# Performance work log

Measured on AMD Instinct MI355X. Metric: run time of the kernel, lower is better.

Reference implementation:

```python
import jax, jax.numpy as jnp
import numpy as np


def _rope(x, token_positions, theta):
    # x: [B, H, S, D], token_positions: [S]
    d = x.shape[-1]
    freqs = 1.0 / theta ** (jnp.arange(0, d, 2, dtype=jnp.float32) / d)  # [D/2]
    angles = token_positions.astype(jnp.float32)[:, None] * freqs[None, :]  # [S, D/2]
    cos, sin = jnp.cos(angles), jnp.sin(angles)
    x_even = x[..., 0::2]
    x_odd = x[..., 1::2]
    new_even = x_even * cos - x_odd * sin
    new_odd = x_even * sin + x_odd * cos
    return jnp.stack([new_even, new_odd], axis=-1).reshape(x.shape)


def setup_inputs() -> dict:
    key = jax.random.key(0)
    ks = jax.random.split(key, 5)
    B, S, D = 2, 2048, 1024
    scale = 1.0 / np.sqrt(D)
    return {
        "x": jax.random.normal(ks[0], (B, S, D), dtype=jnp.float32),
        "Wq": jax.random.normal(ks[1], (D, D), dtype=jnp.float32) * scale,
        "Wk": jax.random.normal(ks[2], (D, D), dtype=jnp.float32) * scale,
        "Wv": jax.random.normal(ks[3], (D, D), dtype=jnp.float32) * scale,
        "Wo": jax.random.normal(ks[4], (D, D), dtype=jnp.float32) * scale,
        "token_positions": jnp.arange(S, dtype=jnp.int32),
        "rope_theta": 10000,
    }


def reference(x, Wq, Wk, Wv, Wo, token_positions, rope_theta):
    B, S, Dm = x.shape
    H = 16
    d_k = Dm // H
    # nn.Linear(bias=False): y = x @ W.T
    def proj(W):
        y = jnp.einsum('bsd,ed->bse', x, W)
        return y.reshape(B, S, H, d_k).transpose(0, 2, 1, 3)  # [B,H,S,Dk]
    q = _rope(proj(Wq), token_positions, float(rope_theta))
    k = _rope(proj(Wk), token_positions, float(rope_theta))
    v = proj(Wv)
    scores = jnp.einsum('bhqd,bhkd->bhqk', q, k) / jnp.sqrt(jnp.float32(d_k))
    causal = jnp.tril(jnp.ones((S, S), dtype=bool))
    scores = jnp.where(causal, scores, -jnp.inf)
    p = jax.nn.softmax(scores, axis=-1)
    vals = jnp.einsum('bhqk,bhkd->bhqd', p, v)
    out = vals.transpose(0, 2, 1, 3).reshape(B, S, Dm)
    return jnp.einsum('bsd,ed->bse', out, Wo)
```

## Files before the change

### kernel.cpp

```cpp
#include <hip/hip_runtime.h>
#include <hip/hip_bf16.h>
#include <stdint.h>

typedef __attribute__((ext_vector_type(8))) __bf16 bf16x8;
typedef __attribute__((ext_vector_type(4))) float f32x4;
typedef __hip_bfloat16 bf16;

#define GLDS(g, l) __builtin_amdgcn_global_load_lds( \
    (const __attribute__((address_space(1))) void*)(g), \
    (__attribute__((address_space(3))) void*)(l), 16, 0, 0)

#define SCALE_Q 0.18033688f
#define MFIX 12.0f

#define OFF_XB     ((size_t)0)
#define OFF_WQKVB  ((size_t)8388608)
#define OFF_WOB    ((size_t)14680064)
#define OFF_QB     ((size_t)16777216)
#define OFF_KB     ((size_t)25165824)
#define OFF_VTB    ((size_t)33554432)
#define OFF_CS     ((size_t)41943040)
#define OFF_SN     ((size_t)42205184)

__global__ void prep_kernel(const float* __restrict__ x, const float* __restrict__ wq,
                            const float* __restrict__ wk, const float* __restrict__ wv,
                            const float* __restrict__ wo,
                            bf16* __restrict__ xb, bf16* __restrict__ wqkvb,
                            bf16* __restrict__ wob,
                            const int* __restrict__ pos, const void* __restrict__ theta_p,
                            float* __restrict__ cst, float* __restrict__ snt)
{
    const int region = blockIdx.y;
    if (region == 5) {
        if (blockIdx.x >= 256) return;
        const int t = blockIdx.x * 256 + threadIdx.x;
        const int s = t >> 5, i = t & 31;
        const int ti = ((const int*)theta_p)[0];
        const float theta = (ti > 0 && ti < 100000000) ? (float)ti : ((const float*)theta_p)[0];
        const float fr = expf(-(float)i * (1.0f / 32.0f) * logf(theta));
        const float ang = (float)pos[s] * fr;
        cst[t] = cosf(ang);
        snt[t] = sinf(ang);
        return;
    }
    const float* src;
    bf16* dst;
    int count;
    switch (region) {
        case 0:  src = x;  dst = xb;              count = 4096 * 1024; break;
        case 1:  src = wq; dst = wqkvb;           count = 1024 * 1024; break;
        case 2:  src = wk; dst = wqkvb + 1048576; count = 1024 * 1024; break;
        case 3:  src = wv; dst = wqkvb + 2097152; count = 1024 * 1024; break;
        default: src = wo; dst = wob;             count = 1024 * 1024; break;
    }
    const int i = (blockIdx.x * 256 + threadIdx.x) * 4;
    if (i >= count) return;
    const float4 v = *(const float4*)(src + i);
    union { bf16 h[4]; short4 s4; } u;
    u.h[0] = __float2bfloat16(v.x);
    u.h[1] = __float2bfloat16(v.y);
    u.h[2] = __float2bfloat16(v.z);
    u.h[3] = __float2bfloat16(v.w);
    *(short4*)(dst + i) = u.s4;
}

template<int MODE, int BM>
__global__ __launch_bounds__(256) void gemm_bt(
    const bf16* __restrict__ A, const bf16* __restrict__ B,
    const int K, const int N,
    float* __restrict__ outf,
    bf16* __restrict__ qb, bf16* __restrict__ kb, bf16* __restrict__ vtb,
    const float* __restrict__ cst, const float* __restrict__ snt)
{
    constexpr int NF = BM / 32;
    constexpr int AG = BM / 64;
    constexpr int ABYTES = BM * 64;
    constexpr int BBYTES = 128 * 64;
    constexpr int DBSZ = 2 * (ABYTES + BBYTES);
    constexpr int TLSZ = (MODE == 0) ? 128 * 130 * 2 : 0;
    constexpr int POOL = DBSZ > TLSZ ? DBSZ : TLSZ;
    __shared__ __align__(16) char smem[POOL];
    const int tid = threadIdx.x;
    const int wave = tid >> 6, lane = tid & 63;
    const int lr = lane & 15, lk = lane >> 4;

    const int nwg = gridDim.x * gridDim.y;
    const int flat = blockIdx.y * gridDim.x + blockIdx.x;
    const int wg = (flat & 7) * (nwg >> 3) + (flat >> 3);
    const int m0 = (wg % gridDim.x) * BM;
    const int n0 = (wg / gridDim.x) * 128;

    const int wm = (wave >> 1) * (BM / 2);
    const int wn = (wave & 1) * 64;
    const int srow = tid >> 2, sseg = tid & 3;
    const int swel = (sseg ^ ((srow + (srow >> 2)) & 3)) * 8;

    f32x4 acc[NF][4] = {};

    const bf16* aRow = A + (size_t)(m0 + srow) * K + swel;
    const bf16* bRow = B + (size_t)(n0 + srow) * K + swel;
    const size_t rowK64 = (size_t)64 * K;

    auto STAGE = [&](int step, int c) {
        char* lA = smem + c * ABYTES + tid * 16;
        char* lB = smem + 2 * ABYTES + c * BBYTES + tid * 16;
        const int off = step * 32;
#pragma unroll
        for (int g = 0; g < AG; ++g)
            GLDS(aRow + off + (size_t)g * rowK64, lA + g * 4096);
#pragma unroll
        for (int g = 0; g < 2; ++g)
            GLDS(bRow + off + (size_t)g * rowK64, lB + g * 4096);
    };

    const int xoff = (lk ^ ((lr + (lr >> 2)) & 3)) << 4;
    const int NSTEP = K >> 5;

    STAGE(0, 0);

    for (int ks = 0; ks < NSTEP; ++ks) {
        const int c = ks & 1;
        if (ks < NSTEP - 1) {
            STAGE(ks + 1, c ^ 1);
            if constexpr (AG == 2) asm volatile("s_waitcnt vmcnt(4)" ::: "memory");
            else                   asm volatile("s_waitcnt vmcnt(3)" ::: "memory");
        } else {
            asm volatile("s_waitcnt vmcnt(0)" ::: "memory");
        }
        __builtin_amdgcn_s_barrier();
        __builtin_amdgcn_sched_barrier(0);
        const char* aBase = smem + c * ABYTES;
        const char* bBase = smem + 2 * ABYTES + c * BBYTES;

        bf16x8 af[NF], bfr[4];
#pragma unroll
        for (int i = 0; i < NF; ++i)
            af[i] = *(const bf16x8*)(aBase + (wm + i * 16 + lr) * 64 + xoff);
#pragma unroll
        for (int j = 0; j < 4; ++j)
            bfr[j] = *(const bf16x8*)(bBase + (wn + j * 16 + lr) * 64 + xoff);
#pragma unroll
        for (int i = 0; i < NF; ++i)
#pragma unroll
            for (int j = 0; j < 4; ++j)
                acc[i][j] = __builtin_amdgcn_mfma_f32_16x16x32_bf16(af[i], bfr[j], acc[i][j], 0, 0, 0);
        __builtin_amdgcn_sched_barrier(0);
        __builtin_amdgcn_s_barrier();
    }

    if constexpr (MODE == 1) {
#pragma unroll
        for (int i = 0; i < NF; ++i)
#pragma unroll
            for (int j = 0; j < 4; ++j)
#pragma unroll
                for (int r = 0; r < 4; ++r) {
                    const int row = m0 + wm + i * 16 + lk * 4 + r;
                    const int col = n0 + wn + j * 16 + lr;
                    outf[(size_t)row * N + col] = acc[i][j][r];
                }
    } else {
        const int matn = n0 >> 10;
        if (matn == 2) {
            bf16* Tl = (bf16*)smem;
#pragma unroll
            for (int i = 0; i < NF; ++i)
#pragma unroll
                for (int j = 0; j < 4; ++j)
#pragma unroll
                    for (int r = 0; r < 4; ++r) {
                        const int trow = wm + i * 16 + lk * 4 + r;
                        const int tcol = wn + j * 16 + lr;
                        Tl[tcol * 130 + trow] = __float2bfloat16(acc[i][j][r]);
                    }
            __syncthreads();
            const int b = m0 >> 11;
            const int s0 = m0 & 2047;
#pragma unroll
            for (int k = 0; k < 8; ++k) {
                const int c = wave * 32 + k * 4 + (lane >> 4);
                const int e = (n0 + c) & 1023;
                const size_t bhi = (size_t)(b * 16 + (e >> 6));
                bf16* dst = vtb + (bhi * 64 + (e & 63)) * 2048 + s0 + lr * 8;
                *(uint4*)dst = *(const uint4*)&Tl[c * 130 + lr * 8];
            }
        } else {
#pragma unroll
            for (int i = 0; i < NF; ++i)
#pragma unroll
                for (int j = 0; j < 4; ++j)
#pragma unroll
                    for (int r = 0; r < 4; ++r) {
                        const int row = m0 + wm + i * 16 + lk * 4 + r;
                        const int col = n0 + wn + j * 16 + lr;
                        float v = acc[i][j][r];
                        float p = __shfl_xor(v, 1);
                        const int e = col & 1023;
                        const int h = e >> 6;
                        const int dd = e & 63;
                        const int b = row >> 11;
                        const int s = row & 2047;
                        const size_t bhi = (size_t)(b * 16 + h);
                        const float cs = cst[s * 32 + (dd >> 1)];
                        const float sn = snt[s * 32 + (dd >> 1)];
                        const float rv = (dd & 1) ? (p * sn + v * cs) : (v * cs - p * sn);
                        if (matn == 0)
                            qb[(bhi * 2048 + s) * 64 + dd] = __float2bfloat16(rv * SCALE_Q);
                        else
                            kb[(bhi * 2048 + s) * 64 + dd] = __float2bfloat16(rv);
                    }
        }
    }
}

__global__ __launch_bounds__(256) void attn_kernel(
    const bf16* __restrict__ qb, const bf16* __restrict__ kb,
    const bf16* __restrict__ vtb, bf16* __restrict__ attnb)
{
    __shared__ __align__(16) bf16 Kl[2][64 * 64];
    __shared__ __align__(16) bf16 Vl[2][64 * 64];
    __shared__ __align__(16) bf16 Pl[4][2][16][72];
    const int tid = threadIdx.x;
    const int wave = tid >> 6, lane = tid & 63;
    const int lr = lane & 15, lk = lane >> 4;
    const int tA = blockIdx.x;
    const int tB = 31 - tA;
    const int bh = blockIdx.y;
    const int qA = tA * 64 + wave * 16;
    const int qB = tB * 64 + wave * 16;

    const bf16* Qp = qb + (size_t)bh * 2048 * 64;
    const bf16* Kp = kb + (size_t)bh * 2048 * 64;
    const bf16* Vp = vtb + (size_t)bh * 64 * 2048;

    const int srow = tid >> 3;
    const int sseg = tid & 7;
    const int sw16 = (sseg ^ (srow & 7)) * 16;
    const char* kg = (const char*)Kp + (size_t)srow * 128 + sw16;
    const char* vg = (const char*)Vp + (size_t)srow * 4096 + sw16;

#define STAGE(kt_, c_) do {                                              \
        const char* kgt = kg + (size_t)(kt_) * 8192;                     \
        GLDS(kgt,              &Kl[c_][0] + tid * 8);                    \
        GLDS(kgt + 32 * 128,   &Kl[c_][0] + 2048 + tid * 8);             \
        const char* vgt = vg + (size_t)(kt_) * 128;                      \
        GLDS(vgt,              &Vl[c_][0] + tid * 8);                    \
        GLDS(vgt + 32 * 4096,  &Vl[c_][0] + 2048 + tid * 8);             \
    } while (0)

    bf16x8 qfA[2], qfB[2];
#pragma unroll
    for (int ks = 0; ks < 2; ++ks) {
        qfA[ks] = *(const bf16x8*)(Qp + (qA + lr) * 64 + ks * 32 + lk * 8);
        qfB[ks] = *(const bf16x8*)(Qp + (qB + lr) * 64 + ks * 32 + lk * 8);
    }

    float sA = 0.f, sB = 0.f;
    f32x4 oA[4] = {}, oB[4] = {};

    STAGE(0, 0);

    const int xoff = (lr & 7) * 8;

    for (int kt = 0; kt <= tB; ++kt) {
        const int c = kt & 1;
        const int kv0 = kt * 64;
        const bool doA = (kt <= tA);
        if (kt < tB) {
            STAGE(kt + 1, c ^ 1);
            asm volatile("s_waitcnt vmcnt(4)" ::: "memory");
        } else {
            asm volatile("s_waitcnt vmcnt(0)" ::: "memory");
        }
        __builtin_amdgcn_s_barrier();
        __builtin_amdgcn_sched_barrier(0);
        const bf16* Kc = &Kl[c][0];
        const bf16* Vc = &Vl[c][0];

        f32x4 scB[4] = {}, scA[4] = {};
#pragma unroll
        for (int ks = 0; ks < 2; ++ks) {
            bf16x8 kf[4];
#pragma unroll
            for (int j = 0; j < 4; ++j)
                kf[j] = *(const bf16x8*)(Kc + (j * 16 + lr) * 64 + ((ks * 32 + lk * 8) ^ xoff));
            __builtin_amdgcn_s_setprio(1);
#pragma unroll
            for (int j = 0; j < 4; ++j)
                scB[j] = __builtin_amdgcn_mfma_f32_16x16x32_bf16(kf[j], qfB[ks], scB[j], 0, 0, 0);
            if (doA) {
#pragma unroll
                for (int j = 0; j < 4; ++j)
                    scA[j] = __builtin_amdgcn_mfma_f32_16x16x32_bf16(kf[j], qfA[ks], scA[j], 0, 0, 0);
            }
            __builtin_amdgcn_s_setprio(0);
        }

        bf16x8 vf[2][4];
#pragma unroll
        for (int ks = 0; ks < 2; ++ks)
#pragma unroll
            for (int j = 0; j < 4; ++j)
                vf[ks][j] = *(const bf16x8*)(Vc + (j * 16 + lr) * 64 + ((ks * 32 + lk * 8) ^ xoff));

        auto smx = [&](f32x4* sc, float& ssum, int qX, bool diag, int st) {
            if (diag) {
#pragma unroll
                for (int j = 0; j < 4; ++j)
#pragma unroll
                    for (int r = 0; r < 4; ++r)
                        if (kv0 + j * 16 + lk * 4 + r > qX + lr) sc[j][r] = -1e30f;
            }
            float l0 = 0.f, l1 = 0.f, l2 = 0.f, l3 = 0.f;
#pragma unroll
            for (int j = 0; j < 4; ++j) {
                float pv[4];
                pv[0] = exp2f(sc[j][0] - MFIX);
                pv[1] = exp2f(sc[j][1] - MFIX);
                pv[2] = exp2f(sc[j][2] - MFIX);
                pv[3] = exp2f(sc[j][3] - MFIX);
                l0 += pv[0]; l1 += pv[1]; l2 += pv[2]; l3 += pv[3];
                union { bf16 h[4]; ushort4 s4; } u;
#pragma unroll
                for (int r = 0; r < 4; ++r) u.h[r] = __float2bfloat16(pv[r]);
                *(ushort4*)(&Pl[wave][st][lr][j * 16 + lk * 4]) = u.s4;
            }
            ssum += (l0 + l1) + (l2 + l3);
        };
        auto pv = [&](f32x4* o, int st) {
#pragma unroll
            for (int ks = 0; ks < 2; ++ks) {
                const bf16x8 pf = *(const bf16x8*)(&Pl[wave][st][lr][ks * 32 + lk * 8]);
                __builtin_amdgcn_s_setprio(1);
#pragma unroll
                for (int j = 0; j < 4; ++j)
                    o[j] = __builtin_amdgcn_mfma_f32_16x16x32_bf16(vf[ks][j], pf, o[j], 0, 0, 0);
                __builtin_amdgcn_s_setprio(0);
            }
        };

        smx(scB, sB, qB, kt == tB, 1);
        if (doA) smx(scA, sA, qA, kt == tA, 0);
        pv(oB, 1);
        if (doA) pv(oA, 0);

        __builtin_amdgcn_sched_barrier(0);
        __builtin_amdgcn_s_barrier();
    }

    const int b = bh >> 4, h = bh & 15;
    auto epi = [&](float ssum, f32x4* o, int qX) {
        float s = ssum;
        s += __shfl_xor(s, 16);
        s += __shfl_xor(s, 32);
        const float inv = 1.0f / s;
        const int qq = qX + lr;
        bf16* dst = attnb + (size_t)(b * 2048 + qq) * 1024 + h * 64 + lk * 4;
#pragma unroll
        for (int j = 0; j < 4; ++j) {
            union { bf16 h4[4]; ushort4 s4; } u;
#pragma unroll
            for (int r = 0; r < 4; ++r) u.h4[r] = __float2bfloat16(o[j][r] * inv);
            *(ushort4*)(dst + j * 16) = u.s4;
        }
    };
    epi(sA, oA, qA);
    epi(sB, oB, qB);
#undef STAGE
}

extern "C" void kernel_launch(void* const* d_in, const int* in_sizes, int n_in,
                              void* d_out, int out_size, void* d_ws, size_t ws_size,
                              hipStream_t stream)
{
    const float* x   = (const float*)d_in[0];
    const float* wq  = (const float*)d_in[1];
    const float* wk  = (const float*)d_in[2];
    const float* wv  = (const float*)d_in[3];
    const float* wo  = (const float*)d_in[4];
    const int*   pos = (const int*)d_in[5];
    const void* theta = d_in[6];

    char* ws = (char*)d_ws;
    bf16* xb    = (bf16*)(ws + OFF_XB);
    bf16* attnb = (bf16*)(ws + OFF_XB);
    bf16* wqkvb = (bf16*)(ws + OFF_WQKVB);
    bf16* wob   = (bf16*)(ws + OFF_WOB);
    bf16* qb    = (bf16*)(ws + OFF_QB);
    bf16* kb    = (bf16*)(ws + OFF_KB);
    bf16* vtb   = (bf16*)(ws + OFF_VTB);
    float* cst  = (float*)(ws + OFF_CS);
    float* snt  = (float*)(ws + OFF_SN);

    prep_kernel<<<dim3(4096, 6), 256, 0, stream>>>(x, wq, wk, wv, wo, xb, wqkvb, wob,
                                                   pos, theta, cst, snt);
    gemm_bt<0, 128><<<dim3(32, 24), 256, 0, stream>>>(xb, wqkvb, 1024, 3072, nullptr,
                                                      qb, kb, vtb, cst, snt);
    attn_kernel<<<dim3(16, 32), 256, 0, stream>>>(qb, kb, vtb, attnb);
    gemm_bt<1, 64><<<dim3(64, 8), 256, 0, stream>>>(attnb, wob, 1024, 1024, (float*)d_out,
                                                    nullptr, nullptr, nullptr, nullptr, nullptr);
}
```

Measured before the change: 131.6 us.

## Switch attention to 32x32x16 MFMA with register-resident P via lane shuffles

Rewrites the attention inner loop to use 32x32x16 bf16 MFMA tiles, packing the two causal-paired query tiles (A and B) into the 32 columns of one MFMA instead of issuing separate 16x16 MFMAs for each. The probability matrix is no longer staged through shared memory. It is packed to bf16 with v_cvt_pk_bf16_f32 and rearranged between lane halves with shuffles. Tile A's columns are masked to zero via a bias once A is past its diagonal, so MFMA work for the masked-out half is still issued. This removes the LDS round-trip and its shared buffer but adds shuffle traffic and more accumulator registers.

```diff
diff --git a/kernel.cpp b/kernel.cpp
--- a/kernel.cpp
+++ b/kernel.cpp
@@ -4,6 +4,7 @@
 
 typedef __attribute__((ext_vector_type(8))) __bf16 bf16x8;
 typedef __attribute__((ext_vector_type(4))) float f32x4;
+typedef __attribute__((ext_vector_type(16))) float f32x16;
 typedef __hip_bfloat16 bf16;
 
 #define GLDS(g, l) __builtin_amdgcn_global_load_lds( \
@@ -21,6 +22,12 @@
 #define OFF_VTB    ((size_t)33554432)
 #define OFF_CS     ((size_t)41943040)
 #define OFF_SN     ((size_t)42205184)
+
+static __device__ __forceinline__ unsigned pkbf(float a, float b) {
+    unsigned r;
+    asm("v_cvt_pk_bf16_f32 %0, %1, %2" : "=v"(r) : "v"(a), "v"(b));
+    return r;
+}
 
 __global__ void prep_kernel(const float* __restrict__ x, const float* __restrict__ wq,
                             const float* __restrict__ wk, const float* __restrict__ wv,
@@ -219,15 +226,14 @@
 {
     __shared__ __align__(16) bf16 Kl[2][64 * 64];
     __shared__ __align__(16) bf16 Vl[2][64 * 64];
-    __shared__ __align__(16) bf16 Pl[4][2][16][72];
     const int tid = threadIdx.x;
     const int wave = tid >> 6, lane = tid & 63;
-    const int lr = lane & 15, lk = lane >> 4;
+    const int c32 = lane & 31, G = lane >> 5;
     const int tA = blockIdx.x;
     const int tB = 31 - tA;
     const int bh = blockIdx.y;
-    const int qA = tA * 64 + wave * 16;
-    const int qB = tB * 64 + wave * 16;
+    const int qrow = (c32 < 16) ? (tB * 64 + wave * 16 + c32)
+                                : (tA * 64 + wave * 16 + c32 - 16);
 
     const bf16* Qp = qb + (size_t)bh * 2048 * 64;
     const bf16* Kp = kb + (size_t)bh * 2048 * 64;
@@ -248,24 +254,21 @@
         GLDS(vgt + 32 * 4096,  &Vl[c_][0] + 2048 + tid * 8);             \
     } while (0)
 
-    bf16x8 qfA[2], qfB[2];
-#pragma unroll
-    for (int ks = 0; ks < 2; ++ks) {
-        qfA[ks] = *(const bf16x8*)(Qp + (qA + lr) * 64 + ks * 32 + lk * 8);
-        qfB[ks] = *(const bf16x8*)(Qp + (qB + lr) * 64 + ks * 32 + lk * 8);
-    }
-
-    float sA = 0.f, sB = 0.f;
-    f32x4 oA[4] = {}, oB[4] = {};
+    bf16x8 qf[4];
+#pragma unroll
+    for (int s = 0; s < 4; ++s)
+        qf[s] = *(const bf16x8*)(Qp + (size_t)qrow * 64 + s * 16 + G * 8);
+
+    float ssum = 0.f;
+    f32x16 o0 = {}, o1 = {};
 
     STAGE(0, 0);
 
-    const int xoff = (lr & 7) * 8;
+    const int x7 = c32 & 7;
 
     for (int kt = 0; kt <= tB; ++kt) {
         const int c = kt & 1;
         const int kv0 = kt * 64;
-        const bool doA = (kt <= tA);
         if (kt < tB) {
             STAGE(kt + 1, c ^ 1);
             asm volatile("s_waitcnt vmcnt(4)" ::: "memory");
@@ -277,95 +280,102 @@
         const bf16* Kc = &Kl[c][0];
         const bf16* Vc = &Vl[c][0];
 
-        f32x4 scB[4] = {}, scA[4] = {};
-#pragma unroll
-        for (int ks = 0; ks < 2; ++ks) {
-            bf16x8 kf[4];
-#pragma unroll
-            for (int j = 0; j < 4; ++j)
-                kf[j] = *(const bf16x8*)(Kc + (j * 16 + lr) * 64 + ((ks * 32 + lk * 8) ^ xoff));
+        bf16x8 kf0[4], kf1[4];
+#pragma unroll
+        for (int s = 0; s < 4; ++s) {
+            const int seg = ((2 * s + G) ^ x7) * 8;
+            kf0[s] = *(const bf16x8*)(Kc + (0 * 32 + c32) * 64 + seg);
+            kf1[s] = *(const bf16x8*)(Kc + (1 * 32 + c32) * 64 + seg);
+        }
+
+        f32x16 p0 = {}, p1 = {};
+        __builtin_amdgcn_s_setprio(1);
+#pragma unroll
+        for (int s = 0; s < 4; ++s) {
+            p0 = __builtin_amdgcn_mfma_f32_32x32x16_bf16(kf0[s], qf[s], p0, 0, 0, 0);
+            p1 = __builtin_amdgcn_mfma_f32_32x32x16_bf16(kf1[s], qf[s], p1, 0, 0, 0);
+        }
+        __builtin_amdgcn_s_setprio(0);
+
+        bf16x8 vf0[4], vf1[4];
+#pragma unroll
+        for (int s = 0; s < 4; ++s) {
+            const int seg = ((2 * s + G) ^ x7) * 8;
+            vf0[s] = *(const bf16x8*)(Vc + (0 * 32 + c32) * 64 + seg);
+            vf1[s] = *(const bf16x8*)(Vc + (1 * 32 + c32) * 64 + seg);
+        }
+
+        if (kt == tA || kt == tB) {
+            const int thr0 = qrow - kv0 - 4 * G;
+            const int thr1 = thr0 - 32;
+#pragma unroll
+            for (int r = 0; r < 16; ++r) {
+                const int cr = (r & 3) + 8 * (r >> 2);
+                if (cr > thr0) p0[r] = -1e30f;
+                if (cr > thr1) p1[r] = -1e30f;
+            }
+        }
+        const float bias = (c32 >= 16 && kt > tA) ? -1e30f : -MFIX;
+
+        float ls = 0.f;
+#pragma unroll
+        for (int r = 0; r < 16; ++r) {
+            p0[r] = exp2f(p0[r] + bias);
+            p1[r] = exp2f(p1[r] + bias);
+            ls += p0[r] + p1[r];
+        }
+        ssum += ls;
+
+#pragma unroll
+        for (int s = 0; s < 4; ++s) {
+            const int sb = (s & 1) * 8;
+            float a0, a1, a2, a3, b0, b1, b2, b3;
+            if (s < 2) {
+                a0 = p0[sb+0]; a1 = p0[sb+1]; a2 = p0[sb+2]; a3 = p0[sb+3];
+                b0 = p0[sb+4]; b1 = p0[sb+5]; b2 = p0[sb+6]; b3 = p0[sb+7];
+            } else {
+                a0 = p1[sb+0]; a1 = p1[sb+1]; a2 = p1[sb+2]; a3 = p1[sb+3];
+                b0 = p1[sb+4]; b1 = p1[sb+5]; b2 = p1[sb+6]; b3 = p1[sb+7];
+            }
+            const unsigned plo0 = pkbf(a0, a1), plo1 = pkbf(a2, a3);
+            const unsigned phi0 = pkbf(b0, b1), phi1 = pkbf(b2, b3);
+            const unsigned send0 = G ? plo0 : phi0;
+            const unsigned send1 = G ? plo1 : phi1;
+            const unsigned recv0 = (unsigned)__shfl_xor((int)send0, 32);
+            const unsigned recv1 = (unsigned)__shfl_xor((int)send1, 32);
+            union { unsigned u[4]; bf16x8 v; } pf;
+            pf.u[0] = G ? recv0 : plo0;
+            pf.u[1] = G ? recv1 : plo1;
+            pf.u[2] = G ? phi0 : recv0;
+            pf.u[3] = G ? phi1 : recv1;
             __builtin_amdgcn_s_setprio(1);
-#pragma unroll
-            for (int j = 0; j < 4; ++j)
-                scB[j] = __builtin_amdgcn_mfma_f32_16x16x32_bf16(kf[j], qfB[ks], scB[j], 0, 0, 0);
-            if (doA) {
-#pragma unroll
-                for (int j = 0; j < 4; ++j)
-                    scA[j] = __builtin_amdgcn_mfma_f32_16x16x32_bf16(kf[j], qfA[ks], scA[j], 0, 0, 0);
-            }
+            o0 = __builtin_amdgcn_mfma_f32_32x32x16_bf16(vf0[s], pf.v, o0, 0, 0, 0);
+            o1 = __builtin_amdgcn_mfma_f32_32x32x16_bf16(vf1[s], pf.v, o1, 0, 0, 0);
             __builtin_amdgcn_s_setprio(0);
         }
-
-        bf16x8 vf[2][4];
-#pragma unroll
-        for (int ks = 0; ks < 2; ++ks)
-#pragma unroll
-            for (int j = 0; j < 4; ++j)
-                vf[ks][j] = *(const bf16x8*)(Vc + (j * 16 + lr) * 64 + ((ks * 32 + lk * 8) ^ xoff));
-
-        auto smx = [&](f32x4* sc, float& ssum, int qX, bool diag, int st) {
-            if (diag) {
-#pragma unroll
-                for (int j = 0; j < 4; ++j)
-#pragma unroll
-                    for (int r = 0; r < 4; ++r)
-                        if (kv0 + j * 16 + lk * 4 + r > qX + lr) sc[j][r] = -1e30f;
-            }
-            float l0 = 0.f, l1 = 0.f, l2 = 0.f, l3 = 0.f;
-#pragma unroll
-            for (int j = 0; j < 4; ++j) {
-                float pv[4];
-                pv[0] = exp2f(sc[j][0] - MFIX);
-                pv[1] = exp2f(sc[j][1] - MFIX);
-                pv[2] = exp2f(sc[j][2] - MFIX);
-                pv[3] = exp2f(sc[j][3] - MFIX);
-                l0 += pv[0]; l1 += pv[1]; l2 += pv[2]; l3 += pv[3];
-                union { bf16 h[4]; ushort4 s4; } u;
-#pragma unroll
-                for (int r = 0; r < 4; ++r) u.h[r] = __float2bfloat16(pv[r]);
-                *(ushort4*)(&Pl[wave][st][lr][j * 16 + lk * 4]) = u.s4;
-            }
-            ssum += (l0 + l1) + (l2 + l3);
-        };
-        auto pv = [&](f32x4* o, int st) {
-#pragma unroll
-            for (int ks = 0; ks < 2; ++ks) {
-                const bf16x8 pf = *(const bf16x8*)(&Pl[wave][st][lr][ks * 32 + lk * 8]);
-                __builtin_amdgcn_s_setprio(1);
-#pragma unroll
-                for (int j = 0; j < 4; ++j)
-                    o[j] = __builtin_amdgcn_mfma_f32_16x16x32_bf16(vf[ks][j], pf, o[j], 0, 0, 0);
-                __builtin_amdgcn_s_setprio(0);
-            }
-        };
-
-        smx(scB, sB, qB, kt == tB, 1);
-        if (doA) smx(scA, sA, qA, kt == tA, 0);
-        pv(oB, 1);
-        if (doA) pv(oA, 0);
 
         __builtin_amdgcn_sched_barrier(0);
         __builtin_amdgcn_s_barrier();
     }
 
     const int b = bh >> 4, h = bh & 15;
-    auto epi = [&](float ssum, f32x4* o, int qX) {
-        float s = ssum;
-        s += __shfl_xor(s, 16);
-        s += __shfl_xor(s, 32);
-        const float inv = 1.0f / s;
-        const int qq = qX + lr;
-        bf16* dst = attnb + (size_t)(b * 2048 + qq) * 1024 + h * 64 + lk * 4;
-#pragma unroll
-        for (int j = 0; j < 4; ++j) {
-            union { bf16 h4[4]; ushort4 s4; } u;
-#pragma unroll
-            for (int r = 0; r < 4; ++r) u.h4[r] = __float2bfloat16(o[j][r] * inv);
-            *(ushort4*)(dst + j * 16) = u.s4;
-        }
-    };
-    epi(sA, oA, qA);
-    epi(sB, oB, qB);
+    const float stot = ssum + __shfl_xor(ssum, 32);
+    const float inv = 1.0f / stot;
+    bf16* dst = attnb + (size_t)(b * 2048 + qrow) * 1024 + h * 64;
+#pragma unroll
+    for (int dt = 0; dt < 2; ++dt) {
+#pragma unroll
+        for (int bq = 0; bq < 4; ++bq) {
+            const int d0 = dt * 32 + 8 * bq + 4 * G;
+            float v0, v1, v2, v3;
+            if (dt == 0) { v0 = o0[4*bq]; v1 = o0[4*bq+1]; v2 = o0[4*bq+2]; v3 = o0[4*bq+3]; }
+            else         { v0 = o1[4*bq]; v1 = o1[4*bq+1]; v2 = o1[4*bq+2]; v3 = o1[4*bq+3]; }
+            uint2 w;
+            w.x = pkbf(v0 * inv, v1 * inv);
+            w.y = pkbf(v2 * inv, v3 * inv);
+            *(uint2*)(dst + d0) = w;
+        }
+    }
 #undef STAGE
 }
 
```

Measured after the change: 157.2 us. 1.2x slower.
